# Performance work log

Hardware: AMD Instinct MI355X
Metric: run time of the kernel (lower is better)

## Reference

```python
import jax, jax.numpy as jnp
import numpy as np

B, S, D, H = 2, 2048, 1024, 16
DH = D // H
DIM_K = 1024


def setup_inputs() -> dict:
    key = jax.random.key(0)
    ks = jax.random.split(key, 5)
    sc = 0.02
    return {
        "x": jax.random.normal(ks[0], (B, S, D), dtype=jnp.float32),
        "Wq": jax.random.normal(ks[1], (D, DIM_K), dtype=jnp.float32) * sc,
        "Wk": jax.random.normal(ks[2], (D, DIM_K), dtype=jnp.float32) * sc,
        "Wv": jax.random.normal(ks[3], (D, DIM_K), dtype=jnp.float32) * sc,
        "Wo": jax.random.normal(ks[4], (DIM_K, DIM_K), dtype=jnp.float32) * sc,
    }


def reference(x, Wq, Wk, Wv, Wo):
    # projections (Linear, no bias); weights stored as [in, out]
    q = (x @ Wq).reshape(B, S, H, DH).transpose(0, 2, 1, 3)  # [B,H,S,DH]
    k = (x @ Wk).reshape(B, S, H, DH).transpose(0, 2, 1, 3)
    v = (x @ Wv).reshape(B, S, H, DH).transpose(0, 2, 1, 3)

    scores = jnp.einsum("bhqd,bhkd->bhqk", q, k)  # [B,H,S,S]
    # causal mask applied BEFORE scaling, as in the original
    causal_mask = jnp.triu(jnp.ones((S, S), dtype=bool), k=1)
    m_inf = -jnp.finfo(scores.dtype).max
    scores = jnp.where(causal_mask[None, None], m_inf, scores)
    attn = jax.nn.softmax(scores * (DIM_K ** -0.5), axis=-1)

    out = jnp.einsum("bhqk,bhkd->bhqd", attn, v)  # [B,H,S,DH]
    out = out.transpose(0, 2, 1, 3).reshape(B, S, DIM_K)
    return out @ Wo
```

## Files before the change

### kernel.cpp

```cpp
#include <hip/hip_runtime.h>


#define AS1 __attribute__((address_space(1)))
#define AS3 __attribute__((address_space(3)))
#define EXPC2 0.04508422f

typedef __attribute__((ext_vector_type(4))) float f32x4;
typedef __attribute__((ext_vector_type(8))) short bf16x8;

__device__ __forceinline__ void gload16(const void* g, void* l) {
  __builtin_amdgcn_global_load_lds((const AS1 unsigned int*)g,
                                   (AS3 unsigned int*)l, 16, 0, 0);
}
__device__ __forceinline__ unsigned short f2b(float f) {
  unsigned u = __float_as_uint(f);
  return (unsigned short)((u + 0x7FFFu + ((u >> 16) & 1u)) >> 16);
}
__device__ __forceinline__ float fexp2(float x) {
  float r;
  asm("v_exp_f32 %0, %1" : "=v"(r) : "v"(x));
  return r;
}
__device__ __forceinline__ unsigned cvtpk(float a, float b) {
  unsigned r;
  asm("v_cvt_pk_bf16_f32 %0, %1, %2" : "=v"(r) : "v"(a), "v"(b));
  return r;
}

__global__ __launch_bounds__(256) void prep(
    const float* __restrict__ x, const float* __restrict__ W0,
    const float* __restrict__ W1, const float* __restrict__ W2,
    const float* __restrict__ W3, unsigned short* __restrict__ xb,
    unsigned short* __restrict__ Wt) {
  __shared__ float T[64][65];
  const int tid = threadIdx.x;
  const int bid = blockIdx.x;
  if (bid < 4096) {
    const size_t i = (size_t)(bid * 256 + tid) * 4;
    float4 v = *(const float4*)&x[i];
    uint2 o;
    o.x = f2b(v.x) | ((unsigned)f2b(v.y) << 16);
    o.y = f2b(v.z) | ((unsigned)f2b(v.w) << 16);
    *(uint2*)&xb[i] = o;
    return;
  }
  const int idx = bid - 4096;
  const int kb = (idx & 15) * 64, nb = ((idx >> 4) & 15) * 64, z = idx >> 8;
  const float* W = (z == 0) ? W0 : (z == 1) ? W1 : (z == 2) ? W2 : W3;
  unsigned short* D = Wt + (size_t)z * 1024 * 1024;
#pragma unroll
  for (int p = 0; p < 4; ++p) {
    const int s = p * 256 + tid;
    const int r = s >> 4, c4 = s & 15;
    float4 v = *(const float4*)&W[(size_t)(kb + r) * 1024 + nb + c4 * 4];
    T[r][c4 * 4 + 0] = v.x;
    T[r][c4 * 4 + 1] = v.y;
    T[r][c4 * 4 + 2] = v.z;
    T[r][c4 * 4 + 3] = v.w;
  }
  __syncthreads();
#pragma unroll
  for (int p = 0; p < 4; ++p) {
    const int s = p * 256 + tid;
    const int n = s >> 4, k4 = s & 15;
    uint2 o;
    o.x = f2b(T[k4 * 4 + 0][n]) | ((unsigned)f2b(T[k4 * 4 + 1][n]) << 16);
    o.y = f2b(T[k4 * 4 + 2][n]) | ((unsigned)f2b(T[k4 * 4 + 3][n]) << 16);
    *(uint2*)&D[(size_t)(nb + n) * 1024 + kb + k4 * 4] = o;
  }
}

__global__ __launch_bounds__(512, 2) void gemm_qkv(
    const unsigned short* __restrict__ xb, const unsigned short* __restrict__ Wt,
    unsigned short* __restrict__ Qb, unsigned short* __restrict__ Kb,
    unsigned short* __restrict__ Vp) {
  __shared__ unsigned short smem[32768];

  const int tid = threadIdx.x, lane = tid & 63, w = tid >> 6;
  const int bm = blockIdx.x / 12, bn = blockIdx.x % 12;
  const int wr = w >> 1, wc = w & 1;

  f32x4 acc[4][8];
#pragma unroll
  for (int m = 0; m < 4; ++m)
#pragma unroll
    for (int n = 0; n < 8; ++n) acc[m][n] = (f32x4)0.0f;

  const int lu = (lane & 7) ^ (lane >> 3);
  const int srow2 = 2 * (lane >> 3) + (lu >> 2);
  const int scol2 = (lu & 3) * 8;
  const int c0 = w * 2, c1 = w * 2 + 1;
  const size_t arow0 = (size_t)(bm * 256 + c0 * 16 + srow2) * 1024 + scol2;
  const size_t arow1 = (size_t)(bm * 256 + c1 * 16 + srow2) * 1024 + scol2;
  const size_t brow0 = (size_t)(bn * 256 + c0 * 16 + srow2) * 1024 + scol2;
  const size_t brow1 = (size_t)(bn * 256 + c1 * 16 + srow2) * 1024 + scol2;

  const int fr = lane & 15, g = lane >> 4;
  const int fh = fr >> 1;
  const int pcx = ((((fr & 1) << 2) | g) ^ fh) * 8;

#define QSTAGE(BUF, KC)                                                      \
  {                                                                          \
    gload16(&xb[arow0 + (KC)], &smem[(BUF)*16384 + c0 * 512]);               \
    gload16(&xb[arow1 + (KC)], &smem[(BUF)*16384 + c1 * 512]);               \
    gload16(&Wt[brow0 + (KC)], &smem[8192 + (BUF)*16384 + c0 * 512]);        \
    gload16(&Wt[brow1 + (KC)], &smem[8192 + (BUF)*16384 + c1 * 512]);        \
  }

  QSTAGE(0, 0)
  int cur = 0;

  for (int t = 0; t < 32; ++t) {
    __syncthreads();
    if (t + 1 < 32) QSTAGE(cur ^ 1, (t + 1) * 32)

    bf16x8 af[4], bf[8];
#pragma unroll
    for (int m = 0; m < 4; ++m)
      af[m] = *(const bf16x8*)&smem[cur * 16384 + (wr * 32 + m * 8 + fh) * 64 +
                                    pcx];
#pragma unroll
    for (int n = 0; n < 8; ++n)
      bf[n] = *(const bf16x8*)&smem[8192 + cur * 16384 +
                                    (wc * 64 + n * 8 + fh) * 64 + pcx];
#pragma unroll
    for (int m = 0; m < 4; ++m)
#pragma unroll
      for (int n = 0; n < 8; ++n)
        acc[m][n] = __builtin_amdgcn_mfma_f32_16x16x32_bf16(af[m], bf[n],
                                                            acc[m][n], 0, 0, 0);
    cur ^= 1;
  }

  const int fq = lane >> 4;
  if (bn < 8) {
    unsigned short* Ob = (bn < 4) ? Qb : Kb;
    const int cbase = (bn & 3) * 256;
#pragma unroll
    for (int mf = 0; mf < 4; ++mf)
#pragma unroll
      for (int nf = 0; nf < 8; ++nf) {
        const int col = cbase + wc * 128 + nf * 16 + fr;
        const int h = col >> 6, d = col & 63;
#pragma unroll
        for (int rr = 0; rr < 4; ++rr) {
          const int m = bm * 256 + wr * 64 + mf * 16 + fq * 4 + rr;
          const int b = m >> 11, s = m & 2047;
          Ob[((size_t)(b * 16 + h) * 2048 + s) * 64 + d] = f2b(acc[mf][nf][rr]);
        }
      }
    return;
  }

  const int chb = (bn - 8) * 256;
  const int s0all = bm * 256;
  const int b = s0all >> 11;
#pragma unroll
  for (int qq = 0; qq < 4; ++qq) {
    const int qm = qq >> 1, qn = qq & 1;
    __syncthreads();
    if (wc == qn && (wr >> 1) == qm) {
#pragma unroll
      for (int mf = 0; mf < 4; ++mf)
#pragma unroll
        for (int nf = 0; nf < 8; ++nf) {
          const int cl = nf * 16 + fr;
#pragma unroll
          for (int rr = 0; rr < 4; ++rr) {
            const int ml = (wr & 1) * 64 + mf * 16 + fq * 4 + rr;
            const int u = ml & 63, a = u >> 4;
            const int sperm = (ml & 64) | ((a >> 1) * 32 + ((u >> 2) & 3) * 8 +
                                           (a & 1) * 4 + (u & 3));
            smem[cl * 132 + sperm] = f2b(acc[mf][nf][rr]);
          }
        }
    }
    __syncthreads();
    const int row = tid >> 2, cg = (tid & 3) * 32;
    const int ch = chb + qn * 128 + row;
    const int h = ch >> 6, d = ch & 63;
    const int sb = (s0all + qm * 128) & 2047;
    unsigned short* dst = &Vp[((size_t)(b * 16 + h) * 64 + d) * 2048 + sb + cg];
    *(uint4*)(dst + 0) = *(const uint4*)&smem[row * 132 + cg];
    *(uint4*)(dst + 8) = *(const uint4*)&smem[row * 132 + cg + 8];
    *(uint4*)(dst + 16) = *(const uint4*)&smem[row * 132 + cg + 16];
    *(uint4*)(dst + 24) = *(const uint4*)&smem[row * 132 + cg + 24];
  }
#undef QSTAGE
}

__global__ __launch_bounds__(256) void gemm_out(
    const unsigned short* __restrict__ A, const unsigned short* __restrict__ B,
    float* __restrict__ Of) {
  __shared__ unsigned short smem[16384];

  const int tid = threadIdx.x, lane = tid & 63, w = tid >> 6;
  const int bm = blockIdx.x >> 3, bn = blockIdx.x & 7;
  const int wr = w >> 1, wc = w & 1;

  f32x4 acc[4][4];
#pragma unroll
  for (int m = 0; m < 4; ++m)
#pragma unroll
    for (int n = 0; n < 4; ++n) acc[m][n] = (f32x4)0.0f;

  const int lu = (lane & 7) ^ (lane >> 3);
  const int srow2 = 2 * (lane >> 3) + (lu >> 2);
  const int scol2 = (lu & 3) * 8;
  const size_t arow = (size_t)(bm * 128 + srow2) * 1024 + scol2;
  const size_t brow = (size_t)(bn * 128 + srow2) * 1024 + scol2;

  const int fr = lane & 15, g = lane >> 4;
  const int fh = fr >> 1;
  const int pcx = ((((fr & 1) << 2) | g) ^ fh) * 8;

#define OSTAGE(BUF, KC)                                                      \
  {                                                                          \
    _Pragma("unroll") for (int q = 0; q < 2; ++q) {                          \
      const int r = w * 32 + q * 16;                                         \
      gload16(&A[arow + (size_t)r * 1024 + (KC)],                            \
              &smem[(BUF) * 8192 + r * 32]);                                 \
      gload16(&B[brow + (size_t)r * 1024 + (KC)],                            \
              &smem[(BUF) * 8192 + 4096 + r * 32]);                          \
    }                                                                        \
  }

  OSTAGE(0, 0)
  int cur = 0;

  for (int t = 0; t < 32; ++t) {
    __syncthreads();
    if (t + 1 < 32) OSTAGE(cur ^ 1, (t + 1) * 32)

    bf16x8 af[4], bf[4];
#pragma unroll
    for (int m = 0; m < 4; ++m)
      af[m] = *(const bf16x8*)&smem[cur * 8192 + (wr * 32 + m * 8 + fh) * 64 +
                                    pcx];
#pragma unroll
    for (int n = 0; n < 4; ++n)
      bf[n] = *(const bf16x8*)&smem[cur * 8192 + 4096 +
                                    (wc * 32 + n * 8 + fh) * 64 + pcx];
#pragma unroll
    for (int m = 0; m < 4; ++m)
#pragma unroll
      for (int n = 0; n < 4; ++n)
        acc[m][n] = __builtin_amdgcn_mfma_f32_16x16x32_bf16(af[m], bf[n],
                                                            acc[m][n], 0, 0, 0);
    cur ^= 1;
  }

  const int fq = lane >> 4;
#pragma unroll
  for (int mf = 0; mf < 4; ++mf)
#pragma unroll
    for (int nf = 0; nf < 4; ++nf) {
      const int col = bn * 128 + wc * 64 + nf * 16 + fr;
#pragma unroll
      for (int rr = 0; rr < 4; ++rr) {
        const int m = bm * 128 + wr * 64 + mf * 16 + fq * 4 + rr;
        Of[(size_t)m * 1024 + col] = acc[mf][nf][rr];
      }
    }
#undef OSTAGE
}

__global__ __launch_bounds__(256) void attn_q64(
    const unsigned short* __restrict__ Qb, const unsigned short* __restrict__ Kb,
    const unsigned short* __restrict__ Vp, unsigned short* __restrict__ Ab) {
  __shared__ unsigned short smem[16384];

  const int tid = threadIdx.x, lane = tid & 63, w = tid >> 6;
  const int lo = lane & 15, hi = lane >> 4;

  const int id = blockIdx.x;
  const int qtr = id >> 8;
  const int g = (id >> 5) & 7;
  const int bh = id & 31;
  const int bq = (qtr == 0)   ? 2 * g
                 : (qtr == 1) ? 2 * g + 1
                 : (qtr == 2) ? 31 - 2 * g
                              : 30 - 2 * g;
  const int qw = bq * 64 + w * 16;
  const size_t base = (size_t)bh * (2048 * 64);

  bf16x8 qf[2];
#pragma unroll
  for (int ks = 0; ks < 2; ++ks)
    qf[ks] =
        *(const bf16x8*)&Qb[base + (size_t)(qw + lo) * 64 + ks * 32 + hi * 8];

  f32x4 accO[4];
#pragma unroll
  for (int mf = 0; mf < 4; ++mf) accO[mf] = (f32x4)0.0f;
  float mrow = -1e30f, lpart = 0.0f;

  const int ntile = bq + 1;
  const unsigned short* kgb = Kb + base;
  const unsigned short* vgb = Vp + base;
  const int lseg = w * 512;

#define STAGE(BUF, KBASE)                                                    \
  {                                                                          \
    const int kb_ = (KBASE);                                                 \
    _Pragma("unroll") for (int qq = 0; qq < 2; ++qq) {                       \
      const int slot = qq * 256 + tid;                                       \
      const int row = slot >> 3, ch = (slot & 7) ^ (row & 7);                \
      gload16(kgb + (size_t)(kb_ + row) * 64 + ch * 8,                       \
              &smem[(BUF)*4096 + qq * 2048 + lseg]);                         \
      gload16(vgb + (size_t)row * 2048 + kb_ + ch * 8,                       \
              &smem[8192 + (BUF)*4096 + qq * 2048 + lseg]);                  \
    }                                                                        \
  }

  STAGE(0, 0)
  int cur = 0;

  for (int t = 0; t < ntile; ++t) {
    __syncthreads();
    if (t + 1 < ntile) STAGE(cur ^ 1, (t + 1) * 64)

    const int kb = t * 64;
    const int x7 = lo & 7;
    bf16x8 ka[2][4];
#pragma unroll
    for (int ks = 0; ks < 2; ++ks) {
      const int ch = (ks * 4 + hi) ^ x7;
#pragma unroll
      for (int kf = 0; kf < 4; ++kf)
        ka[ks][kf] =
            *(const bf16x8*)&smem[cur * 4096 + (kf * 16 + lo) * 64 + ch * 8];
    }
    f32x4 st[4];
#pragma unroll
    for (int kf = 0; kf < 4; ++kf) st[kf] = (f32x4)0.0f;
    __builtin_amdgcn_s_setprio(1);
#pragma unroll
    for (int ks = 0; ks < 2; ++ks)
#pragma unroll
      for (int kf = 0; kf < 4; ++kf)
        st[kf] = __builtin_amdgcn_mfma_f32_16x16x32_bf16(ka[ks][kf], qf[ks],
                                                         st[kf], 0, 0, 0);
    __builtin_amdgcn_s_setprio(0);

    bf16x8 va[2][4];
#pragma unroll
    for (int ks = 0; ks < 2; ++ks) {
      const int ch = (ks * 4 + hi) ^ x7;
#pragma unroll
      for (int mf = 0; mf < 4; ++mf)
        va[ks][mf] = *(const bf16x8*)&smem[8192 + cur * 4096 +
                                           (mf * 16 + lo) * 64 + ch * 8];
    }

    float v[16];
#pragma unroll
    for (int kf = 0; kf < 4; ++kf)
#pragma unroll
      for (int rr = 0; rr < 4; ++rr) v[kf * 4 + rr] = st[kf][rr];
    if (kb + 63 > qw) {
      const int qg = qw + lo;
#pragma unroll
      for (int kf = 0; kf < 4; ++kf)
#pragma unroll
        for (int rr = 0; rr < 4; ++rr)
          if (kb + kf * 16 + hi * 4 + rr > qg) v[kf * 4 + rr] = -1e30f;
    }
    float mx = fmaxf(fmaxf(fmaxf(v[0], v[1]), fmaxf(v[2], v[3])),
                     fmaxf(fmaxf(v[4], v[5]), fmaxf(v[6], v[7])));
    mx = fmaxf(mx, fmaxf(fmaxf(fmaxf(v[8], v[9]), fmaxf(v[10], v[11])),
                         fmaxf(fmaxf(v[12], v[13]), fmaxf(v[14], v[15]))));
    mx = fmaxf(mx, __shfl_xor(mx, 16));
    mx = fmaxf(mx, __shfl_xor(mx, 32));
    if (!__all(mx - mrow <= 64.0f)) {
      const float mnew = fmaxf(mrow, mx);
      const float al = fexp2((mrow - mnew) * EXPC2);
      mrow = mnew;
      lpart *= al;
#pragma unroll
      for (int mf = 0; mf < 4; ++mf)
#pragma unroll
        for (int rr = 0; rr < 4; ++rr) accO[mf][rr] *= al;
    }
    float p[16], rs = 0.0f;
#pragma unroll
    for (int i = 0; i < 16; ++i) {
      p[i] = fexp2((v[i] - mrow) * EXPC2);
      rs += p[i];
    }
    lpart += rs;

    bf16x8 pb[2];
#pragma unroll
    for (int ks = 0; ks < 2; ++ks) {
      uint4 u;
      u.x = cvtpk(p[ks * 8 + 0], p[ks * 8 + 1]);
      u.y = cvtpk(p[ks * 8 + 2], p[ks * 8 + 3]);
      u.z = cvtpk(p[ks * 8 + 4], p[ks * 8 + 5]);
      u.w = cvtpk(p[ks * 8 + 6], p[ks * 8 + 7]);
      pb[ks] = *(bf16x8*)&u;
    }

    __builtin_amdgcn_s_setprio(1);
#pragma unroll
    for (int ks = 0; ks < 2; ++ks)
#pragma unroll
      for (int mf = 0; mf < 4; ++mf)
        accO[mf] = __builtin_amdgcn_mfma_f32_16x16x32_bf16(va[ks][mf], pb[ks],
                                                           accO[mf], 0, 0, 0);
    __builtin_amdgcn_s_setprio(0);
    cur ^= 1;
  }

  __syncthreads();

  float l = lpart;
  l += __shfl_xor(l, 16);
  l += __shfl_xor(l, 32);
  const float linv = 1.0f / l;
  unsigned short* ot = &smem[w * 1152];
#pragma unroll
  for (int mf = 0; mf < 4; ++mf) {
    uint2 u;
    u.x = cvtpk(accO[mf][0] * linv, accO[mf][1] * linv);
    u.y = cvtpk(accO[mf][2] * linv, accO[mf][3] * linv);
    *(uint2*)&ot[lo * 72 + mf * 16 + hi * 4] = u;
  }
  const int b = bh >> 4, h = bh & 15;
  const int row = lane >> 2, cg = (lane & 3) * 16;
  uint4 o0 = *(const uint4*)&ot[row * 72 + cg];
  uint4 o1 = *(const uint4*)&ot[row * 72 + cg + 8];
  unsigned short* op = &Ab[(size_t)(b * 2048 + qw + row) * 1024 + h * 64 + cg];
  *(uint4*)op = o0;
  *(uint4*)(op + 8) = o1;
#undef STAGE
}

extern "C" void kernel_launch(void* const* d_in, const int* in_sizes, int n_in,
                              void* d_out, int out_size, void* d_ws,
                              size_t ws_size, hipStream_t stream) {
  (void)in_sizes; (void)n_in; (void)out_size; (void)ws_size;
  const float* x = (const float*)d_in[0];
  const float* Wq = (const float*)d_in[1];
  const float* Wk = (const float*)d_in[2];
  const float* Wv = (const float*)d_in[3];
  const float* Wo = (const float*)d_in[4];
  float* out = (float*)d_out;

  char* ws = (char*)d_ws;
  unsigned short* xb = (unsigned short*)(ws);
  unsigned short* Wt = (unsigned short*)(ws + (8u << 20));
  unsigned short* Qb = (unsigned short*)(ws + (16u << 20));
  unsigned short* Kb = (unsigned short*)(ws + (24u << 20));
  unsigned short* Vp = (unsigned short*)(ws + (32u << 20));
  unsigned short* Ab = (unsigned short*)(ws + (40u << 20));
  unsigned short* Wto = Wt + (size_t)3 * 1024 * 1024;

  prep<<<dim3(5120), 256, 0, stream>>>(x, Wq, Wk, Wv, Wo, xb, Wt);
  gemm_qkv<<<dim3(192), 512, 0, stream>>>(xb, Wt, Qb, Kb, Vp);
  attn_q64<<<dim3(1024), 256, 0, stream>>>(Qb, Kb, Vp, Ab);
  gemm_out<<<dim3(256), 256, 0, stream>>>(Ab, Wto, out);
}
```

Baseline: 108.1 us.

## Widen attention query tiles to 128 rows and deepen output GEMM K-step

The attention kernel now gives each block 128 query rows, with each wave handling two 16-row query fragments that share one K/V tile load. This halves the block count and doubles K/V reuse from shared memory. Waves past their causal limit skip compute but still join the barriers. The output GEMM now stages K=64 per iteration with XOR-swizzled rows and double the shared memory, halving loop trips and barriers. The risks are more register pressure, fewer blocks to balance the causal workload, and higher LDS use per block.

New measurement: 112.7 us. 1.04x slower.

```diff
diff --git a/kernel.cpp b/kernel.cpp
--- a/kernel.cpp
+++ b/kernel.cpp
@@ -192,7 +192,7 @@
 __global__ __launch_bounds__(256) void gemm_out(
     const unsigned short* __restrict__ A, const unsigned short* __restrict__ B,
     float* __restrict__ Of) {
-  __shared__ unsigned short smem[16384];
+  __shared__ unsigned short smem[32768];
 
   const int tid = threadIdx.x, lane = tid & 63, w = tid >> 6;
   const int bm = blockIdx.x >> 3, bn = blockIdx.x & 7;
@@ -204,49 +204,47 @@
 #pragma unroll
     for (int n = 0; n < 4; ++n) acc[m][n] = (f32x4)0.0f;
 
-  const int lu = (lane & 7) ^ (lane >> 3);
-  const int srow2 = 2 * (lane >> 3) + (lu >> 2);
-  const int scol2 = (lu & 3) * 8;
-  const size_t arow = (size_t)(bm * 128 + srow2) * 1024 + scol2;
-  const size_t brow = (size_t)(bn * 128 + srow2) * 1024 + scol2;
-
   const int fr = lane & 15, g = lane >> 4;
-  const int fh = fr >> 1;
-  const int pcx = ((((fr & 1) << 2) | g) ^ fh) * 8;
+  const int x7 = fr & 7;
 
 #define OSTAGE(BUF, KC)                                                      \
   {                                                                          \
-    _Pragma("unroll") for (int q = 0; q < 2; ++q) {                          \
-      const int r = w * 32 + q * 16;                                         \
-      gload16(&A[arow + (size_t)r * 1024 + (KC)],                            \
-              &smem[(BUF) * 8192 + r * 32]);                                 \
-      gload16(&B[brow + (size_t)r * 1024 + (KC)],                            \
-              &smem[(BUF) * 8192 + 4096 + r * 32]);                          \
+    _Pragma("unroll") for (int p = 0; p < 4; ++p) {                          \
+      const int slot = p * 256 + tid;                                        \
+      const int row = slot >> 3, ch = (slot & 7) ^ (row & 7);                \
+      gload16(&A[(size_t)(bm * 128 + row) * 1024 + (KC) + ch * 8],           \
+              &smem[(BUF)*16384 + (p * 256 + w * 64) * 8]);                  \
+      gload16(&B[(size_t)(bn * 128 + row) * 1024 + (KC) + ch * 8],           \
+              &smem[(BUF)*16384 + 8192 + (p * 256 + w * 64) * 8]);           \
     }                                                                        \
   }
 
   OSTAGE(0, 0)
   int cur = 0;
 
-  for (int t = 0; t < 32; ++t) {
+  for (int t = 0; t < 16; ++t) {
     __syncthreads();
-    if (t + 1 < 32) OSTAGE(cur ^ 1, (t + 1) * 32)
-
-    bf16x8 af[4], bf[4];
-#pragma unroll
-    for (int m = 0; m < 4; ++m)
-      af[m] = *(const bf16x8*)&smem[cur * 8192 + (wr * 32 + m * 8 + fh) * 64 +
-                                    pcx];
-#pragma unroll
-    for (int n = 0; n < 4; ++n)
-      bf[n] = *(const bf16x8*)&smem[cur * 8192 + 4096 +
-                                    (wc * 32 + n * 8 + fh) * 64 + pcx];
-#pragma unroll
-    for (int m = 0; m < 4; ++m)
+    if (t + 1 < 16) OSTAGE(cur ^ 1, (t + 1) * 64)
+
+#pragma unroll
+    for (int ks2 = 0; ks2 < 2; ++ks2) {
+      const int ch = ((ks2 * 4 + g) ^ x7) * 8;
+      bf16x8 af[4], bf[4];
+#pragma unroll
+      for (int m = 0; m < 4; ++m)
+        af[m] = *(const bf16x8*)&smem[cur * 16384 +
+                                      (wr * 64 + m * 16 + fr) * 64 + ch];
 #pragma unroll
       for (int n = 0; n < 4; ++n)
-        acc[m][n] = __builtin_amdgcn_mfma_f32_16x16x32_bf16(af[m], bf[n],
-                                                            acc[m][n], 0, 0, 0);
+        bf[n] = *(const bf16x8*)&smem[cur * 16384 + 8192 +
+                                      (wc * 64 + n * 16 + fr) * 64 + ch];
+#pragma unroll
+      for (int m = 0; m < 4; ++m)
+#pragma unroll
+        for (int n = 0; n < 4; ++n)
+          acc[m][n] = __builtin_amdgcn_mfma_f32_16x16x32_bf16(
+              af[m], bf[n], acc[m][n], 0, 0, 0);
+    }
     cur ^= 1;
   }
 
@@ -265,7 +263,7 @@
 #undef OSTAGE
 }
 
-__global__ __launch_bounds__(256) void attn_q64(
+__global__ __launch_bounds__(256) void attn_q128(
     const unsigned short* __restrict__ Qb, const unsigned short* __restrict__ Kb,
     const unsigned short* __restrict__ Vp, unsigned short* __restrict__ Ab) {
   __shared__ unsigned short smem[16384];
@@ -274,28 +272,30 @@
   const int lo = lane & 15, hi = lane >> 4;
 
   const int id = blockIdx.x;
-  const int qtr = id >> 8;
-  const int g = (id >> 5) & 7;
   const int bh = id & 31;
-  const int bq = (qtr == 0)   ? 2 * g
-                 : (qtr == 1) ? 2 * g + 1
-                 : (qtr == 2) ? 31 - 2 * g
-                              : 30 - 2 * g;
-  const int qw = bq * 64 + w * 16;
+  const int g3 = (id >> 5) & 7;
+  const int bq = (id >> 8) ? (15 - g3) : g3;
+  const int qw = bq * 128 + w * 32;
   const size_t base = (size_t)bh * (2048 * 64);
 
-  bf16x8 qf[2];
-#pragma unroll
-  for (int ks = 0; ks < 2; ++ks)
-    qf[ks] =
-        *(const bf16x8*)&Qb[base + (size_t)(qw + lo) * 64 + ks * 32 + hi * 8];
-
-  f32x4 accO[4];
-#pragma unroll
-  for (int mf = 0; mf < 4; ++mf) accO[mf] = (f32x4)0.0f;
-  float mrow = -1e30f, lpart = 0.0f;
-
-  const int ntile = bq + 1;
+  bf16x8 qf[2][2];
+#pragma unroll
+  for (int qn = 0; qn < 2; ++qn)
+#pragma unroll
+    for (int ks = 0; ks < 2; ++ks)
+      qf[qn][ks] = *(const bf16x8*)&Qb[base +
+                                       (size_t)(qw + qn * 16 + lo) * 64 +
+                                       ks * 32 + hi * 8];
+
+  f32x4 accO[4][2];
+#pragma unroll
+  for (int mf = 0; mf < 4; ++mf)
+#pragma unroll
+    for (int qn = 0; qn < 2; ++qn) accO[mf][qn] = (f32x4)0.0f;
+  float mrow[2] = {-1e30f, -1e30f}, lpart[2] = {0.0f, 0.0f};
+
+  const int ntile = 2 * bq + 2;
+  const int wlast = 2 * bq + (w >> 1);
   const unsigned short* kgb = Kb + base;
   const unsigned short* vgb = Vp + base;
   const int lseg = w * 512;
@@ -320,119 +320,139 @@
     __syncthreads();
     if (t + 1 < ntile) STAGE(cur ^ 1, (t + 1) * 64)
 
-    const int kb = t * 64;
-    const int x7 = lo & 7;
-    bf16x8 ka[2][4];
-#pragma unroll
-    for (int ks = 0; ks < 2; ++ks) {
-      const int ch = (ks * 4 + hi) ^ x7;
+    if (t <= wlast) {
+      const int kb = t * 64;
+      const int x7 = lo & 7;
+      bf16x8 ka[2][4];
+#pragma unroll
+      for (int ks = 0; ks < 2; ++ks) {
+        const int ch = (ks * 4 + hi) ^ x7;
+#pragma unroll
+        for (int kf = 0; kf < 4; ++kf)
+          ka[ks][kf] =
+              *(const bf16x8*)&smem[cur * 4096 + (kf * 16 + lo) * 64 + ch * 8];
+      }
+      f32x4 st[4][2];
 #pragma unroll
       for (int kf = 0; kf < 4; ++kf)
-        ka[ks][kf] =
-            *(const bf16x8*)&smem[cur * 4096 + (kf * 16 + lo) * 64 + ch * 8];
+#pragma unroll
+        for (int qn = 0; qn < 2; ++qn) st[kf][qn] = (f32x4)0.0f;
+      __builtin_amdgcn_s_setprio(1);
+#pragma unroll
+      for (int ks = 0; ks < 2; ++ks)
+#pragma unroll
+        for (int kf = 0; kf < 4; ++kf)
+#pragma unroll
+          for (int qn = 0; qn < 2; ++qn)
+            st[kf][qn] = __builtin_amdgcn_mfma_f32_16x16x32_bf16(
+                ka[ks][kf], qf[qn][ks], st[kf][qn], 0, 0, 0);
+      __builtin_amdgcn_s_setprio(0);
+
+      bf16x8 va[2][4];
+#pragma unroll
+      for (int ks = 0; ks < 2; ++ks) {
+        const int ch = (ks * 4 + hi) ^ x7;
+#pragma unroll
+        for (int mf = 0; mf < 4; ++mf)
+          va[ks][mf] = *(const bf16x8*)&smem[8192 + cur * 4096 +
+                                             (mf * 16 + lo) * 64 + ch * 8];
+      }
+
+      bf16x8 pb[2][2];
+#pragma unroll
+      for (int qn = 0; qn < 2; ++qn) {
+        float v[16];
+#pragma unroll
+        for (int kf = 0; kf < 4; ++kf)
+#pragma unroll
+          for (int rr = 0; rr < 4; ++rr) v[kf * 4 + rr] = st[kf][qn][rr];
+        if (kb + 63 > qw) {
+          const int qg = qw + qn * 16 + lo;
+#pragma unroll
+          for (int kf = 0; kf < 4; ++kf)
+#pragma unroll
+            for (int rr = 0; rr < 4; ++rr)
+              if (kb + kf * 16 + hi * 4 + rr > qg) v[kf * 4 + rr] = -1e30f;
+        }
+        float mx = fmaxf(fmaxf(fmaxf(v[0], v[1]), fmaxf(v[2], v[3])),
+                         fmaxf(fmaxf(v[4], v[5]), fmaxf(v[6], v[7])));
+        mx = fmaxf(mx, fmaxf(fmaxf(fmaxf(v[8], v[9]), fmaxf(v[10], v[11])),
+                             fmaxf(fmaxf(v[12], v[13]), fmaxf(v[14], v[15]))));
+        mx = fmaxf(mx, __shfl_xor(mx, 16));
+        mx = fmaxf(mx, __shfl_xor(mx, 32));
+        if (!__all(mx - mrow[qn] <= 64.0f)) {
+          const float mnew = fmaxf(mrow[qn], mx);
+          const float al = fexp2((mrow[qn] - mnew) * EXPC2);
+          mrow[qn] = mnew;
+          lpart[qn] *= al;
+#pragma unroll
+          for (int mf = 0; mf < 4; ++mf)
+#pragma unroll
+            for (int rr = 0; rr < 4; ++rr) accO[mf][qn][rr] *= al;
+        }
+        float p[16], rs = 0.0f;
+#pragma unroll
+        for (int i = 0; i < 16; ++i) {
+          p[i] = fexp2((v[i] - mrow[qn]) * EXPC2);
+          rs += p[i];
+        }
+        lpart[qn] += rs;
+#pragma unroll
+        for (int ks = 0; ks < 2; ++ks) {
+          uint4 u;
+          u.x = cvtpk(p[ks * 8 + 0], p[ks * 8 + 1]);
+          u.y = cvtpk(p[ks * 8 + 2], p[ks * 8 + 3]);
+          u.z = cvtpk(p[ks * 8 + 4], p[ks * 8 + 5]);
+          u.w = cvtpk(p[ks * 8 + 6], p[ks * 8 + 7]);
+          pb[qn][ks] = *(bf16x8*)&u;
+        }
+      }
+
+      __builtin_amdgcn_s_setprio(1);
+#pragma unroll
+      for (int ks = 0; ks < 2; ++ks)
+#pragma unroll
+        for (int mf = 0; mf < 4; ++mf)
+#pragma unroll
+          for (int qn = 0; qn < 2; ++qn)
+            accO[mf][qn] = __builtin_amdgcn_mfma_f32_16x16x32_bf16(
+                va[ks][mf], pb[qn][ks], accO[mf][qn], 0, 0, 0);
+      __builtin_amdgcn_s_setprio(0);
     }
-    f32x4 st[4];
-#pragma unroll
-    for (int kf = 0; kf < 4; ++kf) st[kf] = (f32x4)0.0f;
-    __builtin_amdgcn_s_setprio(1);
-#pragma unroll
-    for (int ks = 0; ks < 2; ++ks)
-#pragma unroll
-      for (int kf = 0; kf < 4; ++kf)
-        st[kf] = __builtin_amdgcn_mfma_f32_16x16x32_bf16(ka[ks][kf], qf[ks],
-                                                         st[kf], 0, 0, 0);
-    __builtin_amdgcn_s_setprio(0);
-
-    bf16x8 va[2][4];
-#pragma unroll
-    for (int ks = 0; ks < 2; ++ks) {
-      const int ch = (ks * 4 + hi) ^ x7;
-#pragma unroll
-      for (int mf = 0; mf < 4; ++mf)
-        va[ks][mf] = *(const bf16x8*)&smem[8192 + cur * 4096 +
-                                           (mf * 16 + lo) * 64 + ch * 8];
+    cur ^= 1;
+  }
+
+  __syncthreads();
+
+  float linv[2];
+#pragma unroll
+  for (int qn = 0; qn < 2; ++qn) {
+    float l = lpart[qn];
+    l += __shfl_xor(l, 16);
+    l += __shfl_xor(l, 32);
+    linv[qn] = 1.0f / l;
+  }
+  unsigned short* ot = &smem[w * 2304];
+#pragma unroll
+  for (int qn = 0; qn < 2; ++qn)
+#pragma unroll
+    for (int mf = 0; mf < 4; ++mf) {
+      uint2 u;
+      u.x = cvtpk(accO[mf][qn][0] * linv[qn], accO[mf][qn][1] * linv[qn]);
+      u.y = cvtpk(accO[mf][qn][2] * linv[qn], accO[mf][qn][3] * linv[qn]);
+      *(uint2*)&ot[(qn * 16 + lo) * 72 + mf * 16 + hi * 4] = u;
     }
-
-    float v[16];
-#pragma unroll
-    for (int kf = 0; kf < 4; ++kf)
-#pragma unroll
-      for (int rr = 0; rr < 4; ++rr) v[kf * 4 + rr] = st[kf][rr];
-    if (kb + 63 > qw) {
-      const int qg = qw + lo;
-#pragma unroll
-      for (int kf = 0; kf < 4; ++kf)
-#pragma unroll
-        for (int rr = 0; rr < 4; ++rr)
-          if (kb + kf * 16 + hi * 4 + rr > qg) v[kf * 4 + rr] = -1e30f;
-    }
-    float mx = fmaxf(fmaxf(fmaxf(v[0], v[1]), fmaxf(v[2], v[3])),
-                     fmaxf(fmaxf(v[4], v[5]), fmaxf(v[6], v[7])));
-    mx = fmaxf(mx, fmaxf(fmaxf(fmaxf(v[8], v[9]), fmaxf(v[10], v[11])),
-                         fmaxf(fmaxf(v[12], v[13]), fmaxf(v[14], v[15]))));
-    mx = fmaxf(mx, __shfl_xor(mx, 16));
-    mx = fmaxf(mx, __shfl_xor(mx, 32));
-    if (!__all(mx - mrow <= 64.0f)) {
-      const float mnew = fmaxf(mrow, mx);
-      const float al = fexp2((mrow - mnew) * EXPC2);
-      mrow = mnew;
-      lpart *= al;
-#pragma unroll
-      for (int mf = 0; mf < 4; ++mf)
-#pragma unroll
-        for (int rr = 0; rr < 4; ++rr) accO[mf][rr] *= al;
-    }
-    float p[16], rs = 0.0f;
-#pragma unroll
-    for (int i = 0; i < 16; ++i) {
-      p[i] = fexp2((v[i] - mrow) * EXPC2);
-      rs += p[i];
-    }
-    lpart += rs;
-
-    bf16x8 pb[2];
-#pragma unroll
-    for (int ks = 0; ks < 2; ++ks) {
-      uint4 u;
-      u.x = cvtpk(p[ks * 8 + 0], p[ks * 8 + 1]);
-      u.y = cvtpk(p[ks * 8 + 2], p[ks * 8 + 3]);
-      u.z = cvtpk(p[ks * 8 + 4], p[ks * 8 + 5]);
-      u.w = cvtpk(p[ks * 8 + 6], p[ks * 8 + 7]);
-      pb[ks] = *(bf16x8*)&u;
-    }
-
-    __builtin_amdgcn_s_setprio(1);
-#pragma unroll
-    for (int ks = 0; ks < 2; ++ks)
-#pragma unroll
-      for (int mf = 0; mf < 4; ++mf)
-        accO[mf] = __builtin_amdgcn_mfma_f32_16x16x32_bf16(va[ks][mf], pb[ks],
-                                                           accO[mf], 0, 0, 0);
-    __builtin_amdgcn_s_setprio(0);
-    cur ^= 1;
-  }
-
-  __syncthreads();
-
-  float l = lpart;
-  l += __shfl_xor(l, 16);
-  l += __shfl_xor(l, 32);
-  const float linv = 1.0f / l;
-  unsigned short* ot = &smem[w * 1152];
-#pragma unroll
-  for (int mf = 0; mf < 4; ++mf) {
-    uint2 u;
-    u.x = cvtpk(accO[mf][0] * linv, accO[mf][1] * linv);
-    u.y = cvtpk(accO[mf][2] * linv, accO[mf][3] * linv);
-    *(uint2*)&ot[lo * 72 + mf * 16 + hi * 4] = u;
-  }
   const int b = bh >> 4, h = bh & 15;
-  const int row = lane >> 2, cg = (lane & 3) * 16;
+  const int row = lane >> 1, cg = (lane & 1) * 32;
   uint4 o0 = *(const uint4*)&ot[row * 72 + cg];
   uint4 o1 = *(const uint4*)&ot[row * 72 + cg + 8];
+  uint4 o2 = *(const uint4*)&ot[row * 72 + cg + 16];
+  uint4 o3 = *(const uint4*)&ot[row * 72 + cg + 24];
   unsigned short* op = &Ab[(size_t)(b * 2048 + qw + row) * 1024 + h * 64 + cg];
-  *(uint4*)op = o0;
+  *(uint4*)(op + 0) = o0;
   *(uint4*)(op + 8) = o1;
+  *(uint4*)(op + 16) = o2;
+  *(uint4*)(op + 24) = o3;
 #undef STAGE
 }
 
@@ -458,6 +478,6 @@
 
   prep<<<dim3(5120), 256, 0, stream>>>(x, Wq, Wk, Wv, Wo, xb, Wt);
   gemm_qkv<<<dim3(192), 512, 0, stream>>>(xb, Wt, Qb, Kb, Vp);
-  attn_q64<<<dim3(1024), 256, 0, stream>>>(Qb, Kb, Vp, Ab);
+  attn_q128<<<dim3(512), 256, 0, stream>>>(Qb, Kb, Vp, Ab);
   gemm_out<<<dim3(256), 256, 0, stream>>>(Ab, Wto, out);
 }
```

## Deepen K-tiles and hand-schedule pipelined loads in QKV and output GEMMs

Applied to the files above, without the earlier changes.

The QKV projection GEMM now stages 64-wide K chunks in two sub-phases with explicit vmcnt waits, raw s_barrier, sched_barriers and setprio around the MFMA block. This lets global-to-LDS loads for the next chunk overlap with compute and halves the number of barrier iterations. The block-to-tile mapping and warp layout also change (bm fastest, 2x4 warps owning 128x64). The output GEMM switches to 64-wide K stages with a new XOR-swizzled LDS layout. LDS use doubles per block, which may reduce occupancy, and the hand-written vmcnt counts must match the number of issued loads exactly.

Result: faster. 101.0 us (-6.5%).

```diff
diff --git a/kernel.cpp b/kernel.cpp
--- a/kernel.cpp
+++ b/kernel.cpp
@@ -74,77 +74,88 @@
     const unsigned short* __restrict__ xb, const unsigned short* __restrict__ Wt,
     unsigned short* __restrict__ Qb, unsigned short* __restrict__ Kb,
     unsigned short* __restrict__ Vp) {
-  __shared__ unsigned short smem[32768];
+  __shared__ unsigned short smem[65536];
 
   const int tid = threadIdx.x, lane = tid & 63, w = tid >> 6;
-  const int bm = blockIdx.x / 12, bn = blockIdx.x % 12;
-  const int wr = w >> 1, wc = w & 1;
-
-  f32x4 acc[4][8];
-#pragma unroll
-  for (int m = 0; m < 4; ++m)
-#pragma unroll
-    for (int n = 0; n < 8; ++n) acc[m][n] = (f32x4)0.0f;
-
-  const int lu = (lane & 7) ^ (lane >> 3);
-  const int srow2 = 2 * (lane >> 3) + (lu >> 2);
-  const int scol2 = (lu & 3) * 8;
-  const int c0 = w * 2, c1 = w * 2 + 1;
-  const size_t arow0 = (size_t)(bm * 256 + c0 * 16 + srow2) * 1024 + scol2;
-  const size_t arow1 = (size_t)(bm * 256 + c1 * 16 + srow2) * 1024 + scol2;
-  const size_t brow0 = (size_t)(bn * 256 + c0 * 16 + srow2) * 1024 + scol2;
-  const size_t brow1 = (size_t)(bn * 256 + c1 * 16 + srow2) * 1024 + scol2;
+  const int bm = blockIdx.x & 15, bn = blockIdx.x >> 4;
+  const int wr = w >> 2, wc = w & 3;
+
+  f32x4 acc[8][4];
+#pragma unroll
+  for (int m = 0; m < 8; ++m)
+#pragma unroll
+    for (int n = 0; n < 4; ++n) acc[m][n] = (f32x4)0.0f;
+
+  const int prow0 = tid >> 3, pc0 = tid & 7;
+  const int u0 = pc0 ^ (prow0 & 7);
+  const int aRow0 = bm * 256 + 2 * prow0 + (u0 >> 2);
+  const int bRow0 = bn * 256 + 2 * prow0 + (u0 >> 2);
+  const int cOff = (u0 & 3) * 8;
 
   const int fr = lane & 15, g = lane >> 4;
-  const int fh = fr >> 1;
-  const int pcx = ((((fr & 1) << 2) | g) ^ fh) * 8;
-
-#define QSTAGE(BUF, KC)                                                      \
-  {                                                                          \
-    gload16(&xb[arow0 + (KC)], &smem[(BUF)*16384 + c0 * 512]);               \
-    gload16(&xb[arow1 + (KC)], &smem[(BUF)*16384 + c1 * 512]);               \
-    gload16(&Wt[brow0 + (KC)], &smem[8192 + (BUF)*16384 + c0 * 512]);        \
-    gload16(&Wt[brow1 + (KC)], &smem[8192 + (BUF)*16384 + c1 * 512]);        \
-  }
-
-  QSTAGE(0, 0)
-  int cur = 0;
-
-  for (int t = 0; t < 32; ++t) {
-    __syncthreads();
-    if (t + 1 < 32) QSTAGE(cur ^ 1, (t + 1) * 32)
-
-    bf16x8 af[4], bf[8];
-#pragma unroll
-    for (int m = 0; m < 4; ++m)
-      af[m] = *(const bf16x8*)&smem[cur * 16384 + (wr * 32 + m * 8 + fh) * 64 +
-                                    pcx];
-#pragma unroll
-    for (int n = 0; n < 8; ++n)
-      bf[n] = *(const bf16x8*)&smem[8192 + cur * 16384 +
-                                    (wc * 64 + n * 8 + fh) * 64 + pcx];
-#pragma unroll
-    for (int m = 0; m < 4; ++m)
-#pragma unroll
-      for (int n = 0; n < 8; ++n)
-        acc[m][n] = __builtin_amdgcn_mfma_f32_16x16x32_bf16(af[m], bf[n],
-                                                            acc[m][n], 0, 0, 0);
-    cur ^= 1;
-  }
-
-  const int fq = lane >> 4;
+  const int frh = fr >> 1;
+  const int pcx = ((((fr & 1) << 2) | g) ^ frh) * 8;
+
+#define STAGE8(BUF, KS, KC)                                                   \
+  {                                                                           \
+    const size_t ko = (size_t)(KC) + (KS)*32 + cOff;                          \
+    gload16(&xb[(size_t)aRow0 * 1024 + ko],                                   \
+            &smem[(BUF)*32768 + (KS)*8192 + tid * 8]);                        \
+    gload16(&xb[(size_t)(aRow0 + 128) * 1024 + ko],                           \
+            &smem[(BUF)*32768 + (KS)*8192 + 4096 + tid * 8]);                 \
+    gload16(&Wt[(size_t)bRow0 * 1024 + ko],                                   \
+            &smem[(BUF)*32768 + 16384 + (KS)*8192 + tid * 8]);                \
+    gload16(&Wt[(size_t)(bRow0 + 128) * 1024 + ko],                           \
+            &smem[(BUF)*32768 + 16384 + (KS)*8192 + 4096 + tid * 8]);         \
+  }
+
+#define PHASE(CUR, KS, VMSTR, STAGESTMT)                                      \
+  {                                                                           \
+    asm volatile(VMSTR ::: "memory");                                         \
+    __builtin_amdgcn_sched_barrier(0);                                        \
+    __builtin_amdgcn_s_barrier();                                             \
+    __builtin_amdgcn_sched_barrier(0);                                        \
+    bf16x8 af[8], bf[4];                                                      \
+    const unsigned short* Ab_ = &smem[(CUR)*32768 + (KS)*8192];               \
+    const unsigned short* Bb_ = &smem[(CUR)*32768 + 16384 + (KS)*8192];       \
+    _Pragma("unroll") for (int mf = 0; mf < 8; ++mf) af[mf] =                 \
+        *(const bf16x8*)&Ab_[(wr * 64 + mf * 8 + frh) * 64 + pcx];            \
+    _Pragma("unroll") for (int nf = 0; nf < 4; ++nf) bf[nf] =                 \
+        *(const bf16x8*)&Bb_[(wc * 32 + nf * 8 + frh) * 64 + pcx];            \
+    STAGESTMT;                                                                \
+    __builtin_amdgcn_s_setprio(1);                                            \
+    _Pragma("unroll") for (int mf = 0; mf < 8; ++mf)                          \
+        _Pragma("unroll") for (int nf = 0; nf < 4; ++nf) acc[mf][nf] =        \
+            __builtin_amdgcn_mfma_f32_16x16x32_bf16(af[mf], bf[nf],           \
+                                                    acc[mf][nf], 0, 0, 0);    \
+    __builtin_amdgcn_s_setprio(0);                                            \
+  }
+
+  STAGE8(0, 0, 0)
+  STAGE8(0, 1, 0)
+
+#pragma unroll 1
+  for (int t = 0; t < 15; ++t) {
+    const int cu_ = t & 1, nb_ = (t + 1) & 1;
+    const int kc1 = (t + 1) * 64;
+    PHASE(cu_, 0, "s_waitcnt vmcnt(4)", STAGE8(nb_, 0, kc1))
+    PHASE(cu_, 1, "s_waitcnt vmcnt(4)", STAGE8(nb_, 1, kc1))
+  }
+  PHASE(1, 0, "s_waitcnt vmcnt(4)", (void)0)
+  PHASE(1, 1, "s_waitcnt vmcnt(0)", (void)0)
+
   if (bn < 8) {
     unsigned short* Ob = (bn < 4) ? Qb : Kb;
     const int cbase = (bn & 3) * 256;
 #pragma unroll
-    for (int mf = 0; mf < 4; ++mf)
-#pragma unroll
-      for (int nf = 0; nf < 8; ++nf) {
-        const int col = cbase + wc * 128 + nf * 16 + fr;
+    for (int mf = 0; mf < 8; ++mf)
+#pragma unroll
+      for (int nf = 0; nf < 4; ++nf) {
+        const int col = cbase + wc * 64 + nf * 16 + fr;
         const int h = col >> 6, d = col & 63;
 #pragma unroll
         for (int rr = 0; rr < 4; ++rr) {
-          const int m = bm * 256 + wr * 64 + mf * 16 + fq * 4 + rr;
+          const int m = bm * 256 + wr * 128 + mf * 16 + g * 4 + rr;
           const int b = m >> 11, s = m & 2047;
           Ob[((size_t)(b * 16 + h) * 2048 + s) * 64 + d] = f2b(acc[mf][nf][rr]);
         }
@@ -159,15 +170,15 @@
   for (int qq = 0; qq < 4; ++qq) {
     const int qm = qq >> 1, qn = qq & 1;
     __syncthreads();
-    if (wc == qn && (wr >> 1) == qm) {
-#pragma unroll
-      for (int mf = 0; mf < 4; ++mf)
-#pragma unroll
-        for (int nf = 0; nf < 8; ++nf) {
-          const int cl = nf * 16 + fr;
+    if (wr == qm && (wc >> 1) == qn) {
+#pragma unroll
+      for (int mf = 0; mf < 8; ++mf)
+#pragma unroll
+        for (int nf = 0; nf < 4; ++nf) {
+          const int cl = (wc & 1) * 64 + nf * 16 + fr;
 #pragma unroll
           for (int rr = 0; rr < 4; ++rr) {
-            const int ml = (wr & 1) * 64 + mf * 16 + fq * 4 + rr;
+            const int ml = mf * 16 + g * 4 + rr;
             const int u = ml & 63, a = u >> 4;
             const int sperm = (ml & 64) | ((a >> 1) * 32 + ((u >> 2) & 3) * 8 +
                                            (a & 1) * 4 + (u & 3));
@@ -186,13 +197,14 @@
     *(uint4*)(dst + 16) = *(const uint4*)&smem[row * 132 + cg + 16];
     *(uint4*)(dst + 24) = *(const uint4*)&smem[row * 132 + cg + 24];
   }
-#undef QSTAGE
+#undef PHASE
+#undef STAGE8
 }
 
 __global__ __launch_bounds__(256) void gemm_out(
     const unsigned short* __restrict__ A, const unsigned short* __restrict__ B,
     float* __restrict__ Of) {
-  __shared__ unsigned short smem[16384];
+  __shared__ unsigned short smem[32768];
 
   const int tid = threadIdx.x, lane = tid & 63, w = tid >> 6;
   const int bm = blockIdx.x >> 3, bn = blockIdx.x & 7;
@@ -204,49 +216,47 @@
 #pragma unroll
     for (int n = 0; n < 4; ++n) acc[m][n] = (f32x4)0.0f;
 
-  const int lu = (lane & 7) ^ (lane >> 3);
-  const int srow2 = 2 * (lane >> 3) + (lu >> 2);
-  const int scol2 = (lu & 3) * 8;
-  const size_t arow = (size_t)(bm * 128 + srow2) * 1024 + scol2;
-  const size_t brow = (size_t)(bn * 128 + srow2) * 1024 + scol2;
-
   const int fr = lane & 15, g = lane >> 4;
-  const int fh = fr >> 1;
-  const int pcx = ((((fr & 1) << 2) | g) ^ fh) * 8;
+  const int x7 = fr & 7;
 
 #define OSTAGE(BUF, KC)                                                      \
   {                                                                          \
-    _Pragma("unroll") for (int q = 0; q < 2; ++q) {                          \
-      const int r = w * 32 + q * 16;                                         \
-      gload16(&A[arow + (size_t)r * 1024 + (KC)],                            \
-              &smem[(BUF) * 8192 + r * 32]);                                 \
-      gload16(&B[brow + (size_t)r * 1024 + (KC)],                            \
-              &smem[(BUF) * 8192 + 4096 + r * 32]);                          \
+    _Pragma("unroll") for (int p = 0; p < 4; ++p) {                          \
+      const int slot = p * 256 + tid;                                        \
+      const int row = slot >> 3, ch = (slot & 7) ^ (row & 7);                \
+      gload16(&A[(size_t)(bm * 128 + row) * 1024 + (KC) + ch * 8],           \
+              &smem[(BUF)*16384 + (p * 256 + w * 64) * 8]);                  \
+      gload16(&B[(size_t)(bn * 128 + row) * 1024 + (KC) + ch * 8],           \
+              &smem[(BUF)*16384 + 8192 + (p * 256 + w * 64) * 8]);           \
     }                                                                        \
   }
 
   OSTAGE(0, 0)
   int cur = 0;
 
-  for (int t = 0; t < 32; ++t) {
+  for (int t = 0; t < 16; ++t) {
     __syncthreads();
-    if (t + 1 < 32) OSTAGE(cur ^ 1, (t + 1) * 32)
-
-    bf16x8 af[4], bf[4];
-#pragma unroll
-    for (int m = 0; m < 4; ++m)
-      af[m] = *(const bf16x8*)&smem[cur * 8192 + (wr * 32 + m * 8 + fh) * 64 +
-                                    pcx];
-#pragma unroll
-    for (int n = 0; n < 4; ++n)
-      bf[n] = *(const bf16x8*)&smem[cur * 8192 + 4096 +
-                                    (wc * 32 + n * 8 + fh) * 64 + pcx];
-#pragma unroll
-    for (int m = 0; m < 4; ++m)
+    if (t + 1 < 16) OSTAGE(cur ^ 1, (t + 1) * 64)
+
+#pragma unroll
+    for (int ks2 = 0; ks2 < 2; ++ks2) {
+      const int ch = ((ks2 * 4 + g) ^ x7) * 8;
+      bf16x8 af[4], bf[4];
+#pragma unroll
+      for (int m = 0; m < 4; ++m)
+        af[m] = *(const bf16x8*)&smem[cur * 16384 +
+                                      (wr * 64 + m * 16 + fr) * 64 + ch];
 #pragma unroll
       for (int n = 0; n < 4; ++n)
-        acc[m][n] = __builtin_amdgcn_mfma_f32_16x16x32_bf16(af[m], bf[n],
-                                                            acc[m][n], 0, 0, 0);
+        bf[n] = *(const bf16x8*)&smem[cur * 16384 + 8192 +
+                                      (wc * 64 + n * 16 + fr) * 64 + ch];
+#pragma unroll
+      for (int m = 0; m < 4; ++m)
+#pragma unroll
+        for (int n = 0; n < 4; ++n)
+          acc[m][n] = __builtin_amdgcn_mfma_f32_16x16x32_bf16(
+              af[m], bf[n], acc[m][n], 0, 0, 0);
+    }
     cur ^= 1;
   }
 
```
